# Kernel tuning notes

Measured on AMD Instinct MI355X. Metric: run time of the kernel, lower is better.

Reference implementation:

```python
import jax, jax.numpy as jnp
import numpy as np

DIM = 1024
SRC_DIM = 1152
NUM_HEADS = 16
HEAD_DIM = DIM // NUM_HEADS  # 64
ROPE_BASE = 10000.0


def rope_tables(seq_len, head_dim):
    # matches RotaryPositionEmbedding: inv_freq over even indices, emb = cat([freqs, freqs])
    inv_freq = 1.0 / (ROPE_BASE ** (jnp.arange(0, head_dim, 2, dtype=jnp.float32) / head_dim))
    t = jnp.arange(seq_len, dtype=jnp.float32)
    freqs = t[:, None] * inv_freq[None, :]          # (L, D/2)
    emb = jnp.concatenate([freqs, freqs], axis=-1)  # (L, D)
    return jnp.cos(emb), jnp.sin(emb)


def rotate_half(x):
    # interleaved rotation as in the torch code
    x1 = x[..., ::2]
    x2 = x[..., 1::2]
    return jnp.stack((-x2, x1), axis=-1).reshape(x.shape)


def apply_rope(t, cos, sin):
    # t: (B, H, L, D); cos/sin: (L, D)
    return t * cos[None, None] + rotate_half(t) * sin[None, None]


def setup_inputs() -> dict:
    key = jax.random.key(0)
    ks = jax.random.split(key, 10)
    B, T, K = 2, 2048, 2048
    s_q = 1.0 / np.sqrt(DIM)
    s_kv = 1.0 / np.sqrt(SRC_DIM)
    return {
        "x": jax.random.normal(ks[0], (B, T, DIM), jnp.float32),
        "context": jax.random.normal(ks[1], (B, K, SRC_DIM), jnp.float32),
        "Wq": jax.random.normal(ks[2], (DIM, DIM), jnp.float32) * s_q,
        "bq": jnp.zeros((DIM,), jnp.float32),
        "Wk": jax.random.normal(ks[3], (DIM, SRC_DIM), jnp.float32) * s_kv,
        "bk": jnp.zeros((DIM,), jnp.float32),
        "Wv": jax.random.normal(ks[4], (DIM, SRC_DIM), jnp.float32) * s_kv,
        "bv": jnp.zeros((DIM,), jnp.float32),
        "Wo": jax.random.normal(ks[5], (DIM, DIM), jnp.float32) * s_q,
        "bo": jnp.zeros((DIM,), jnp.float32),
    }


def reference(x, context, Wq, bq, Wk, bk, Wv, bv, Wo, bo):
    B, T, C = x.shape
    K = context.shape[1]
    H, D = NUM_HEADS, HEAD_DIM

    q = x @ Wq.T + bq                 # (B, T, C)
    k = context @ Wk.T + bk           # (B, K, C)
    v = context @ Wv.T + bv           # (B, K, C)

    q = q.reshape(B, T, H, D).transpose(0, 2, 1, 3)  # (B, H, T, D)
    k = k.reshape(B, K, H, D).transpose(0, 2, 1, 3)  # (B, H, K, D)
    v = v.reshape(B, K, H, D).transpose(0, 2, 1, 3)

    cos_q, sin_q = rope_tables(T, D)
    cos_k, sin_k = rope_tables(K, D)
    q = apply_rope(q, cos_q, sin_q)
    k = apply_rope(k, cos_k, sin_k)

    scale = 1.0 / np.sqrt(D).astype(np.float32)
    scores = jnp.einsum('bhtd,bhkd->bhtk', q, k) * scale  # (B, H, T, K)
    weights = jax.nn.softmax(scores, axis=-1)
    out = jnp.einsum('bhtk,bhkd->bhtd', weights, v)        # (B, H, T, D)
    out = out.transpose(0, 2, 1, 3).reshape(B, T, C)
    return out @ Wo.T + bo
```

## Files before the change

### kernel.cpp

```cpp
#include <hip/hip_runtime.h>
#include <hip/hip_bf16.h>
#include <stdint.h>

typedef unsigned short u16;
typedef __attribute__((ext_vector_type(8))) short bf16x8;
typedef __attribute__((ext_vector_type(8))) unsigned short u16x8;
typedef __attribute__((ext_vector_type(4))) float f32x4;

#define BM 128
#define BN 128
#define BK 32
#define QSCALE 0.18033688f

__device__ __forceinline__ u16 f2bf(float f) {
    union { float f; uint32_t u; } v; v.f = f;
    uint32_t r = v.u + 0x7FFFu + ((v.u >> 16) & 1u);
    return (u16)(r >> 16);
}

__device__ __forceinline__ uint32_t cvt_pk_bf16(float lo, float hi) {
    uint32_t r;
    asm("v_cvt_pk_bf16_f32 %0, %1, %2" : "=v"(r) : "v"(lo), "v"(hi));
    return r;
}

__device__ __forceinline__ float fexp2(float x) {
    float r;
    asm volatile("v_exp_f32 %0, %1\n\ts_nop 0" : "=v"(r) : "v"(x));
    return r;
}

__device__ __forceinline__ void gload_lds16(const void* g, void* l) {
    __builtin_amdgcn_global_load_lds(
        (const __attribute__((address_space(1))) void*)(g),
        (__attribute__((address_space(3))) void*)(l),
        16, 0, 0);
}

__global__ void prep_kernel(const float* __restrict__ x, const float* __restrict__ ctx,
                            const float* __restrict__ Wq, const float* __restrict__ Wk,
                            const float* __restrict__ Wv, const float* __restrict__ Wo,
                            u16* __restrict__ xb, u16* __restrict__ cb,
                            u16* __restrict__ wqb, u16* __restrict__ wkb,
                            u16* __restrict__ wvb, u16* __restrict__ wob,
                            float2* __restrict__ cs) {
    int t = blockIdx.x * 256 + threadIdx.x;
    if (t < 3342336) {
        const float* src; u16* dst; int base;
        if      (t < 1048576) { src = x;   dst = xb;  base = 0; }
        else if (t < 2228224) { src = ctx; dst = cb;  base = 1048576; }
        else if (t < 2490368) { src = Wq;  dst = wqb; base = 2228224; }
        else if (t < 2785280) { src = Wk;  dst = wkb; base = 2490368; }
        else if (t < 3080192) { src = Wv;  dst = wvb; base = 2785280; }
        else                  { src = Wo;  dst = wob; base = 3080192; }
        int i = (t - base) * 4;
        float4 v = *reinterpret_cast<const float4*>(src + i);
        ushort4 o = { f2bf(v.x), f2bf(v.y), f2bf(v.z), f2bf(v.w) };
        *reinterpret_cast<ushort4*>(dst + i) = o;
    } else {
        int idx = t - 3342336;
        int tt = idx >> 5, j = idx & 31;
        float invf = 1.0f / powf(10000.0f, (float)(2 * j) / 64.0f);
        float ang = (float)tt * invf;
        cs[idx] = make_float2(cosf(ang), sinf(ang));
    }
}

__global__ __launch_bounds__(256, 2)
void qkv_gemm(const u16* __restrict__ xb, const u16* __restrict__ cb,
              const u16* __restrict__ wqb, const u16* __restrict__ wkb,
              const u16* __restrict__ wvb,
              const float* __restrict__ bq, const float* __restrict__ bk,
              const float* __restrict__ bv,
              u16* __restrict__ qo, u16* __restrict__ ko, u16* __restrict__ vo,
              const float2* __restrict__ cs)
{
    __shared__ __align__(16) u16 As[BM * BK];
    __shared__ __align__(16) u16 Bs[BN * BK];
    const int bid = blockIdx.x;
    const int seg = bid >> 8, inner = bid & 255;
    const u16* A; const u16* Bm; const float* bias; u16* C;
    int N, K, mbase, nbase, rope, brow;
    float oscale;
    if (seg == 0)      { A = xb;  Bm = wqb; bias = bq; C = qo; N = 1024; K = 1024; rope = 1; brow = 0; oscale = QSCALE; nbase = (inner & 7) * BN;  mbase = (inner >> 3) * BM; }
    else if (seg == 1) { A = cb;  Bm = wkb; bias = bk; C = ko; N = 1024; K = 1152; rope = 1; brow = 0; oscale = 1.0f;   nbase = (inner & 7) * BN;  mbase = (inner >> 3) * BM; }
    else               { A = wvb; Bm = cb;  bias = bv; C = vo; N = 4096; K = 1152; rope = 0; brow = 1; oscale = 1.0f;   nbase = (inner & 31) * BN; mbase = (inner >> 5) * BM; }

    const int tid = threadIdx.x;
    const int wid = tid >> 6, lane = tid & 63;
    const int wr = wid >> 1, wc = wid & 1;
    const int l15 = lane & 15, l4 = lane >> 4;
    const int srow = lane >> 2;
    const int scol = (lane & 3) * 8;

    f32x4 acc[4][4];
#pragma unroll
    for (int i = 0; i < 4; i++)
#pragma unroll
        for (int j = 0; j < 4; j++) acc[i][j] = (f32x4){0.f, 0.f, 0.f, 0.f};

    for (int k0 = 0; k0 < K; k0 += BK) {
#pragma unroll
        for (int q = 0; q < 2; ++q) {
            int segr = wid * 2 + q;
            int row = segr * 16 + srow;
            gload_lds16(A  + (size_t)(mbase + row) * K + k0 + scol, (void*)(As + segr * 512));
            gload_lds16(Bm + (size_t)(nbase + row) * K + k0 + scol, (void*)(Bs + segr * 512));
        }
        __syncthreads();
        bf16x8 af[4], bfv[4];
#pragma unroll
        for (int i = 0; i < 4; i++)
            af[i] = *(const bf16x8*)(As + (wr * 64 + i * 16 + l15) * BK + l4 * 8);
#pragma unroll
        for (int j = 0; j < 4; j++)
            bfv[j] = *(const bf16x8*)(Bs + (wc * 64 + j * 16 + l15) * BK + l4 * 8);
#pragma unroll
        for (int i = 0; i < 4; i++)
#pragma unroll
            for (int j = 0; j < 4; j++)
                acc[i][j] = __builtin_amdgcn_mfma_f32_16x16x32_bf16(af[i], bfv[j], acc[i][j], 0, 0, 0);
        __syncthreads();
    }

#pragma unroll
    for (int i = 0; i < 4; i++) {
#pragma unroll
        for (int j = 0; j < 4; j++) {
#pragma unroll
            for (int r = 0; r < 4; r++) {
                int row = mbase + wr * 64 + i * 16 + l4 * 4 + r;
                int col = nbase + wc * 64 + j * 16 + l15;
                float v = acc[i][j][r] + (brow ? bias[row] : bias[col]);
                if (rope) {
                    float part = __shfl_xor(v, 1);
                    float2 c2 = cs[(row & 2047) * 32 + (col & 31)];
                    v = v * c2.x + ((col & 1) ? part * c2.y : -part * c2.y);
                    v *= oscale;
                }
                C[(size_t)row * N + col] = f2bf(v);
            }
        }
    }
}

__global__ __launch_bounds__(256, 2)
void gemm_out(const u16* __restrict__ A, const u16* __restrict__ B,
              const float* __restrict__ bias, float* __restrict__ C,
              int M, int N, int K)
{
    __shared__ __align__(16) u16 As[BM * BK];
    __shared__ __align__(16) u16 Bs[64 * BK];
    const int tid = threadIdx.x;
    const int wid = tid >> 6, lane = tid & 63;
    const int wr = wid >> 1, wc = wid & 1;
    const int l15 = lane & 15, l4 = lane >> 4;
    const int mbase = blockIdx.y * BM, nbase = blockIdx.x * 64;
    const int srow = lane >> 2;
    const int scol = (lane & 3) * 8;

    f32x4 acc[4][2];
#pragma unroll
    for (int i = 0; i < 4; i++)
#pragma unroll
        for (int j = 0; j < 2; j++) acc[i][j] = (f32x4){0.f, 0.f, 0.f, 0.f};

    for (int k0 = 0; k0 < K; k0 += BK) {
#pragma unroll
        for (int q = 0; q < 2; ++q) {
            int seg = wid * 2 + q;
            int row = seg * 16 + srow;
            gload_lds16(A + (size_t)(mbase + row) * K + k0 + scol, (void*)(As + seg * 512));
        }
        {
            int row = wid * 16 + srow;
            gload_lds16(B + (size_t)(nbase + row) * K + k0 + scol, (void*)(Bs + wid * 512));
        }
        __syncthreads();
        bf16x8 af[4], bfv[2];
#pragma unroll
        for (int i = 0; i < 4; i++)
            af[i] = *(const bf16x8*)(As + (wr * 64 + i * 16 + l15) * BK + l4 * 8);
#pragma unroll
        for (int j = 0; j < 2; j++)
            bfv[j] = *(const bf16x8*)(Bs + (wc * 32 + j * 16 + l15) * BK + l4 * 8);
#pragma unroll
        for (int i = 0; i < 4; i++)
#pragma unroll
            for (int j = 0; j < 2; j++)
                acc[i][j] = __builtin_amdgcn_mfma_f32_16x16x32_bf16(af[i], bfv[j], acc[i][j], 0, 0, 0);
        __syncthreads();
    }

#pragma unroll
    for (int i = 0; i < 4; i++)
#pragma unroll
        for (int j = 0; j < 2; j++)
#pragma unroll
            for (int r = 0; r < 4; r++) {
                int row = mbase + wr * 64 + i * 16 + l4 * 4 + r;
                int col = nbase + wc * 32 + j * 16 + l15;
                C[(size_t)row * N + col] = acc[i][j][r] + bias[col];
            }
}

__device__ __forceinline__ int invrow(int R) {
    return 32 * (R >> 5) + 8 * ((R >> 2) & 3) + 4 * ((R >> 4) & 1) + (R & 3);
}

__global__ __launch_bounds__(256, 4)
void attn_kernel(const u16* __restrict__ Qb, const u16* __restrict__ Kb,
                 const u16* __restrict__ VT, u16* __restrict__ Ob)
{
    const int qt = blockIdx.x;
    const int bh = blockIdx.y;
    const int b = bh >> 4, h = bh & 15;
    __shared__ __align__(16) u16 Ks[2][4096];
    __shared__ __align__(16) u16 Vs[2][4096];
    const int tid = threadIdx.x, wv = tid >> 6, lane = tid & 63;
    const int l15 = lane & 15, l4 = lane >> 4;

    const int r8 = lane >> 3;
    const int cp = lane & 7;
    const int cl = cp ^ r8;
    const int L0 = 2 * wv, L1 = 2 * wv + 1;
    const int RK0 = L0 * 8 + r8, RK1 = L1 * 8 + r8;
    const u16* ksrc0 = Kb + (size_t)(b * 2048 + invrow(RK0)) * 1024 + h * 64 + cl * 8;
    const u16* ksrc1 = Kb + (size_t)(b * 2048 + invrow(RK1)) * 1024 + h * 64 + cl * 8;
    const u16* vsrc0 = VT + (size_t)(h * 64 + RK0) * 4096 + b * 2048 + cl * 8;
    const u16* vsrc1 = VT + (size_t)(h * 64 + RK1) * 4096 + b * 2048 + cl * 8;

    const u16* qrow = Qb + (size_t)(b * 2048 + qt * 64 + wv * 16 + l15) * 1024 + h * 64;
    bf16x8 qf0 = *(const bf16x8*)(qrow + l4 * 8);
    bf16x8 qf1 = *(const bf16x8*)(qrow + 32 + l4 * 8);

    const int swz = l15 & 7;
    const int q0o = (l4 ^ swz) * 8;
    const int q1o = ((4 + l4) ^ swz) * 8;

    f32x4 accO[4];
    float denom = 0.f;
#pragma unroll
    for (int i = 0; i < 4; i++) accO[i] = (f32x4){0.f, 0.f, 0.f, 0.f};

    auto stage = [&](int bs, int kt) {
        gload_lds16(ksrc0 + (size_t)kt * 65536, (void*)&Ks[bs][L0 * 512]);
        gload_lds16(ksrc1 + (size_t)kt * 65536, (void*)&Ks[bs][L1 * 512]);
        gload_lds16(vsrc0 + kt * 64,            (void*)&Vs[bs][L0 * 512]);
        gload_lds16(vsrc1 + kt * 64,            (void*)&Vs[bs][L1 * 512]);
    };

    stage(0, 0);
    __syncthreads();

    int buf = 0;
    for (int kt = 0; kt < 32; ++kt) {
        if (kt < 31) stage(buf ^ 1, kt + 1);

        f32x4 s[4];
#pragma unroll
        for (int j = 0; j < 4; j++) s[j] = (f32x4){0.f, 0.f, 0.f, 0.f};
        __builtin_amdgcn_s_setprio(1);
#pragma unroll
        for (int j = 0; j < 4; j++) {
            const u16* rp = &Ks[buf][(j * 16 + l15) * 64];
            bf16x8 a0 = *(const bf16x8*)(rp + q0o);
            bf16x8 a1 = *(const bf16x8*)(rp + q1o);
            s[j] = __builtin_amdgcn_mfma_f32_16x16x32_bf16(a0, qf0, s[j], 0, 0, 0);
            s[j] = __builtin_amdgcn_mfma_f32_16x16x32_bf16(a1, qf1, s[j], 0, 0, 0);
        }
        __builtin_amdgcn_s_setprio(0);

        float p[4][4];
        float rs = 0.f;
#pragma unroll
        for (int j = 0; j < 4; j++)
#pragma unroll
            for (int r = 0; r < 4; r++) {
                p[j][r] = fexp2(s[j][r]);
                rs += p[j][r];
            }
        rs += __shfl_xor(rs, 16);
        rs += __shfl_xor(rs, 32);
        denom += rs;

        union { uint32_t u[4]; bf16x8 v; } B0u, B1u;
        B0u.u[0] = cvt_pk_bf16(p[0][0], p[0][1]);
        B0u.u[1] = cvt_pk_bf16(p[0][2], p[0][3]);
        B0u.u[2] = cvt_pk_bf16(p[1][0], p[1][1]);
        B0u.u[3] = cvt_pk_bf16(p[1][2], p[1][3]);
        B1u.u[0] = cvt_pk_bf16(p[2][0], p[2][1]);
        B1u.u[1] = cvt_pk_bf16(p[2][2], p[2][3]);
        B1u.u[2] = cvt_pk_bf16(p[3][0], p[3][1]);
        B1u.u[3] = cvt_pk_bf16(p[3][2], p[3][3]);

        __builtin_amdgcn_s_setprio(1);
#pragma unroll
        for (int i = 0; i < 4; i++) {
            const u16* vp = &Vs[buf][(i * 16 + l15) * 64];
            bf16x8 v0 = *(const bf16x8*)(vp + q0o);
            bf16x8 v1 = *(const bf16x8*)(vp + q1o);
            accO[i] = __builtin_amdgcn_mfma_f32_16x16x32_bf16(v0, B0u.v, accO[i], 0, 0, 0);
            accO[i] = __builtin_amdgcn_mfma_f32_16x16x32_bf16(v1, B1u.v, accO[i], 0, 0, 0);
        }
        __builtin_amdgcn_s_setprio(0);
        __syncthreads();
        buf ^= 1;
    }

    float rd = 1.0f / denom;
    u16* orow = Ob + (size_t)(b * 2048 + qt * 64 + wv * 16 + l15) * 1024 + h * 64;
#pragma unroll
    for (int i = 0; i < 4; i++) {
        uint2 st;
        st.x = cvt_pk_bf16(accO[i][0] * rd, accO[i][1] * rd);
        st.y = cvt_pk_bf16(accO[i][2] * rd, accO[i][3] * rd);
        *(uint2*)(orow + i * 16 + l4 * 4) = st;
    }
}

extern "C" void kernel_launch(void* const* d_in, const int* in_sizes, int n_in,
                              void* d_out, int out_size, void* d_ws, size_t ws_size,
                              hipStream_t stream) {
    const float* x   = (const float*)d_in[0];
    const float* ctx = (const float*)d_in[1];
    const float* Wq  = (const float*)d_in[2];
    const float* bq  = (const float*)d_in[3];
    const float* Wk  = (const float*)d_in[4];
    const float* bk  = (const float*)d_in[5];
    const float* Wv  = (const float*)d_in[6];
    const float* bv  = (const float*)d_in[7];
    const float* Wo  = (const float*)d_in[8];
    const float* bo  = (const float*)d_in[9];
    float* out = (float*)d_out;

    char* ws = (char*)d_ws;
    size_t off = 0;
    auto alloc = [&](size_t bytes) { void* p = ws + off; off += (bytes + 255) & ~255ULL; return p; };
    u16* x_bf  = (u16*)alloc(4096ULL * 1024 * 2);
    u16* c_bf  = (u16*)alloc(4096ULL * 1152 * 2);
    u16* wq_bf = (u16*)alloc(1024ULL * 1024 * 2);
    u16* wk_bf = (u16*)alloc(1024ULL * 1152 * 2);
    u16* wv_bf = (u16*)alloc(1024ULL * 1152 * 2);
    u16* wo_bf = (u16*)alloc(1024ULL * 1024 * 2);
    float2* cs = (float2*)alloc(2048ULL * 32 * 8);
    u16* q_bf  = (u16*)alloc(4096ULL * 1024 * 2);
    u16* k_bf  = (u16*)alloc(4096ULL * 1024 * 2);
    u16* vT    = (u16*)alloc(1024ULL * 4096 * 2);
    u16* a_bf  = (u16*)alloc(4096ULL * 1024 * 2);

    prep_kernel<<<13312, 256, 0, stream>>>(x, ctx, Wq, Wk, Wv, Wo,
                                           x_bf, c_bf, wq_bf, wk_bf, wv_bf, wo_bf, cs);
    qkv_gemm<<<768, 256, 0, stream>>>(x_bf, c_bf, wq_bf, wk_bf, wv_bf,
                                      bq, bk, bv, q_bf, k_bf, vT, cs);
    attn_kernel<<<dim3(32, 32), 256, 0, stream>>>(q_bf, k_bf, vT, a_bf);
    gemm_out<<<dim3(16, 32), 256, 0, stream>>>(a_bf, wo_bf, bo, out, 4096, 1024, 1024);
}
```

Measured before the change: 142.6 us.

## Double-buffer LDS tiles in QKV and output GEMMs, swizzle block order

```diff
diff --git a/kernel.cpp b/kernel.cpp
--- a/kernel.cpp
+++ b/kernel.cpp
@@ -75,16 +75,18 @@
               u16* __restrict__ qo, u16* __restrict__ ko, u16* __restrict__ vo,
               const float2* __restrict__ cs)
 {
-    __shared__ __align__(16) u16 As[BM * BK];
-    __shared__ __align__(16) u16 Bs[BN * BK];
+    __shared__ __align__(16) u16 As[2][BM * BK];
+    __shared__ __align__(16) u16 Bs[2][BN * BK];
     const int bid = blockIdx.x;
-    const int seg = bid >> 8, inner = bid & 255;
+    const int wg = (bid & 7) * 96 + (bid >> 3);
+    const int seg = wg >> 8, inner = wg & 255;
     const u16* A; const u16* Bm; const float* bias; u16* C;
     int N, K, mbase, nbase, rope, brow;
     float oscale;
     if (seg == 0)      { A = xb;  Bm = wqb; bias = bq; C = qo; N = 1024; K = 1024; rope = 1; brow = 0; oscale = QSCALE; nbase = (inner & 7) * BN;  mbase = (inner >> 3) * BM; }
     else if (seg == 1) { A = cb;  Bm = wkb; bias = bk; C = ko; N = 1024; K = 1152; rope = 1; brow = 0; oscale = 1.0f;   nbase = (inner & 7) * BN;  mbase = (inner >> 3) * BM; }
     else               { A = wvb; Bm = cb;  bias = bv; C = vo; N = 4096; K = 1152; rope = 0; brow = 1; oscale = 1.0f;   nbase = (inner & 31) * BN; mbase = (inner >> 5) * BM; }
+    const int nk = K >> 5;
 
     const int tid = threadIdx.x;
     const int wid = tid >> 6, lane = tid & 63;
@@ -99,28 +101,35 @@
 #pragma unroll
         for (int j = 0; j < 4; j++) acc[i][j] = (f32x4){0.f, 0.f, 0.f, 0.f};
 
-    for (int k0 = 0; k0 < K; k0 += BK) {
+    auto stage = [&](int bs, int k0) {
 #pragma unroll
         for (int q = 0; q < 2; ++q) {
             int segr = wid * 2 + q;
             int row = segr * 16 + srow;
-            gload_lds16(A  + (size_t)(mbase + row) * K + k0 + scol, (void*)(As + segr * 512));
-            gload_lds16(Bm + (size_t)(nbase + row) * K + k0 + scol, (void*)(Bs + segr * 512));
-        }
-        __syncthreads();
+            gload_lds16(A  + (size_t)(mbase + row) * K + k0 + scol, (void*)(&As[bs][segr * 512]));
+            gload_lds16(Bm + (size_t)(nbase + row) * K + k0 + scol, (void*)(&Bs[bs][segr * 512]));
+        }
+    };
+
+    stage(0, 0);
+    __syncthreads();
+    int buf = 0;
+    for (int ks = 0; ks < nk; ++ks) {
+        if (ks + 1 < nk) stage(buf ^ 1, (ks + 1) * BK);
         bf16x8 af[4], bfv[4];
 #pragma unroll
         for (int i = 0; i < 4; i++)
-            af[i] = *(const bf16x8*)(As + (wr * 64 + i * 16 + l15) * BK + l4 * 8);
+            af[i] = *(const bf16x8*)(&As[buf][(wr * 64 + i * 16 + l15) * BK + l4 * 8]);
 #pragma unroll
         for (int j = 0; j < 4; j++)
-            bfv[j] = *(const bf16x8*)(Bs + (wc * 64 + j * 16 + l15) * BK + l4 * 8);
+            bfv[j] = *(const bf16x8*)(&Bs[buf][(wc * 64 + j * 16 + l15) * BK + l4 * 8]);
 #pragma unroll
         for (int i = 0; i < 4; i++)
 #pragma unroll
             for (int j = 0; j < 4; j++)
                 acc[i][j] = __builtin_amdgcn_mfma_f32_16x16x32_bf16(af[i], bfv[j], acc[i][j], 0, 0, 0);
         __syncthreads();
+        buf ^= 1;
     }
 
 #pragma unroll
@@ -149,8 +158,8 @@
               const float* __restrict__ bias, float* __restrict__ C,
               int M, int N, int K)
 {
-    __shared__ __align__(16) u16 As[BM * BK];
-    __shared__ __align__(16) u16 Bs[64 * BK];
+    __shared__ __align__(16) u16 As[2][BM * BK];
+    __shared__ __align__(16) u16 Bs[2][64 * BK];
     const int tid = threadIdx.x;
     const int wid = tid >> 6, lane = tid & 63;
     const int wr = wid >> 1, wc = wid & 1;
@@ -158,6 +167,7 @@
     const int mbase = blockIdx.y * BM, nbase = blockIdx.x * 64;
     const int srow = lane >> 2;
     const int scol = (lane & 3) * 8;
+    const int nk = K >> 5;
 
     f32x4 acc[4][2];
 #pragma unroll
@@ -165,31 +175,38 @@
 #pragma unroll
         for (int j = 0; j < 2; j++) acc[i][j] = (f32x4){0.f, 0.f, 0.f, 0.f};
 
-    for (int k0 = 0; k0 < K; k0 += BK) {
+    auto stage = [&](int bs, int k0) {
 #pragma unroll
         for (int q = 0; q < 2; ++q) {
             int seg = wid * 2 + q;
             int row = seg * 16 + srow;
-            gload_lds16(A + (size_t)(mbase + row) * K + k0 + scol, (void*)(As + seg * 512));
+            gload_lds16(A + (size_t)(mbase + row) * K + k0 + scol, (void*)(&As[bs][seg * 512]));
         }
         {
             int row = wid * 16 + srow;
-            gload_lds16(B + (size_t)(nbase + row) * K + k0 + scol, (void*)(Bs + wid * 512));
-        }
-        __syncthreads();
+            gload_lds16(B + (size_t)(nbase + row) * K + k0 + scol, (void*)(&Bs[bs][wid * 512]));
+        }
+    };
+
+    stage(0, 0);
+    __syncthreads();
+    int buf = 0;
+    for (int ks = 0; ks < nk; ++ks) {
+        if (ks + 1 < nk) stage(buf ^ 1, (ks + 1) * BK);
         bf16x8 af[4], bfv[2];
 #pragma unroll
         for (int i = 0; i < 4; i++)
-            af[i] = *(const bf16x8*)(As + (wr * 64 + i * 16 + l15) * BK + l4 * 8);
+            af[i] = *(const bf16x8*)(&As[buf][(wr * 64 + i * 16 + l15) * BK + l4 * 8]);
 #pragma unroll
         for (int j = 0; j < 2; j++)
-            bfv[j] = *(const bf16x8*)(Bs + (wc * 32 + j * 16 + l15) * BK + l4 * 8);
+            bfv[j] = *(const bf16x8*)(&Bs[buf][(wc * 32 + j * 16 + l15) * BK + l4 * 8]);
 #pragma unroll
         for (int i = 0; i < 4; i++)
 #pragma unroll
             for (int j = 0; j < 2; j++)
                 acc[i][j] = __builtin_amdgcn_mfma_f32_16x16x32_bf16(af[i], bfv[j], acc[i][j], 0, 0, 0);
         __syncthreads();
+        buf ^= 1;
     }
 
 #pragma unroll
```

Result: no change. 141.7 us (-0.7%).
